# Kernel tuning notes

Measured on AMD Instinct MI355X. Metric: run time of the kernel, lower is better.

## Reference

```python
import math
import jax, jax.numpy as jnp
import numpy as np

N_HEADS = 16

def setup_inputs() -> dict:
    key = jax.random.key(0)
    k1, k2, k3 = jax.random.split(key, 3)
    B, S, D = 2, 2048, 1024
    x = jax.random.normal(k1, (B, S, D), dtype=jnp.float32)
    W_qkv = jax.random.normal(k2, (3 * D, D), dtype=jnp.float32)
    W_o = jax.random.normal(k3, (D, D), dtype=jnp.float32)
    return {"x": x, "W_qkv": W_qkv, "W_o": W_o}


def reference(x, W_qkv, W_o):
    B, S, D = x.shape
    H = N_HEADS
    d_h = D // H
    # fused QKV projection: (B,S,3D)
    t = jnp.matmul(x, W_qkv.T)
    t = t.reshape(B, S, 3, D)
    # NOTE: module reshapes (B,S,D) -> (B,H,S,d_h) directly (no transpose);
    # heads partition the flattened seq*feature layout. Replicate exactly.
    q = t[:, :, 0, :].reshape(B, H, S, d_h)
    k = t[:, :, 1, :].reshape(B, H, S, d_h)
    v = t[:, :, 2, :].reshape(B, H, S, d_h)
    # scaled by sqrt(d_model), as in the original (not sqrt(d_h))
    scores = jnp.einsum('bhqd,bhkd->bhqk', q, k) / math.sqrt(D)
    scores = jnp.tril(scores)
    # original sets ALL exact zeros to -inf (masks upper triangle)
    scores = jnp.where(scores == 0, -jnp.inf, scores)
    attn = jax.nn.softmax(scores, axis=-1)
    y_prime = jnp.matmul(attn, v)  # (B,H,S,d_h)
    y_prime = y_prime.transpose(0, 2, 1, 3).reshape(B, S, D)
    y = jnp.matmul(y_prime, W_o.T)
    return y
```

## Files before the change

kernel.cpp:

```cpp
#include <hip/hip_runtime.h>
#include <hip/hip_bf16.h>


using bf16 = __hip_bfloat16;
typedef __attribute__((ext_vector_type(8))) short bf16x8v;
typedef __attribute__((ext_vector_type(4))) float f32x4;

#define MFMA_BF16(A, B, C) __builtin_amdgcn_mfma_f32_16x16x32_bf16((A), (B), (C), 0, 0, 0)

#define GLD_LDS16(g, l)                                                        \
  __builtin_amdgcn_global_load_lds(                                            \
      (const __attribute__((address_space(1))) void*)(g),                      \
      (__attribute__((address_space(3))) void*)(l), 16, 0, 0)

static __device__ __forceinline__ unsigned short bf_bits(float f) {
  bf16 b = __float2bfloat16(f);
  return *reinterpret_cast<unsigned short*>(&b);
}

__global__ __launch_bounds__(256) void cvt_split(const float* __restrict__ in,
                                                 bf16* __restrict__ hi,
                                                 bf16* __restrict__ lo, int n) {
  int i = (blockIdx.x * 256 + threadIdx.x) * 4;
  if (i >= n) return;
  const float4 v = *(const float4*)(in + i);
  float vv[4] = {v.x, v.y, v.z, v.w};
  ushort4 hb, lb;
  unsigned short* hp = &hb.x;
  unsigned short* lp = &lb.x;
#pragma unroll
  for (int j = 0; j < 4; ++j) {
    bf16 h = __float2bfloat16(vv[j]);
    float r = vv[j] - __bfloat162float(h);
    hp[j] = bf_bits(vv[j]);
    lp[j] = bf_bits(r);
  }
  *(ushort4*)(hi + i) = hb;
  *(ushort4*)(lo + i) = lb;
}

__global__ __launch_bounds__(256) void cvt_plain(const float* __restrict__ in,
                                                 bf16* __restrict__ out, int n) {
  int i = (blockIdx.x * 256 + threadIdx.x) * 4;
  if (i >= n) return;
  const float4 v = *(const float4*)(in + i);
  ushort4 ob;
  ob.x = bf_bits(v.x); ob.y = bf_bits(v.y); ob.z = bf_bits(v.z); ob.w = bf_bits(v.w);
  *(ushort4*)(out + i) = ob;
}

__global__ __launch_bounds__(256) void gemm_qkv(
    const bf16* __restrict__ Ah, const bf16* __restrict__ Al,
    const bf16* __restrict__ Bh, const bf16* __restrict__ Bl,
    bf16* __restrict__ Qhi, bf16* __restrict__ Qlo,
    bf16* __restrict__ Khi, bf16* __restrict__ Klo,
    bf16* __restrict__ Vt) {
  const int K = 1024;
  const int NT = 24;
  __shared__ __attribute__((aligned(16))) bf16 AsH[2][4096], AsL[2][4096],
                                               BsH[2][4096], BsL[2][4096];
  const int t = threadIdx.x;
  const int lane = t & 63;
  const int wave = t >> 6;
  const int wr = wave >> 1, wc = wave & 1;
  int bid = blockIdx.x;
  bid = (bid & 7) * (768 >> 3) + (bid >> 3);
  const int bm = bid / NT, bn = bid % NT;
  const int brow = bm * 128, bcol = bn * 128;
  const bool isV = (bcol >= 2048);
  const bf16* pAh = Ah + (size_t)brow * K;
  const bf16* pAl = Al + (size_t)brow * K;
  const bf16* pBh = Bh + (size_t)bcol * K;
  const bf16* pBl = Bl + (size_t)bcol * K;
  const int r0 = t >> 2;
  const int c0 = (t & 3) * 8;
  f32x4 acc[4][4] = {};

#define STAGE(buf, k0_)                                                        \
  {                                                                            \
    const int _k = (k0_);                                                      \
    GLD_LDS16(pAh + (size_t)r0 * K + _k + c0,        &AsH[buf][t * 8]);        \
    GLD_LDS16(pAh + (size_t)(r0 + 64) * K + _k + c0, &AsH[buf][2048 + t * 8]); \
    GLD_LDS16(pBh + (size_t)r0 * K + _k + c0,        &BsH[buf][t * 8]);        \
    GLD_LDS16(pBh + (size_t)(r0 + 64) * K + _k + c0, &BsH[buf][2048 + t * 8]); \
    if (!isV) {                                                                \
      GLD_LDS16(pAl + (size_t)r0 * K + _k + c0,        &AsL[buf][t * 8]);      \
      GLD_LDS16(pAl + (size_t)(r0 + 64) * K + _k + c0, &AsL[buf][2048 + t * 8]);\
      GLD_LDS16(pBl + (size_t)r0 * K + _k + c0,        &BsL[buf][t * 8]);      \
      GLD_LDS16(pBl + (size_t)(r0 + 64) * K + _k + c0, &BsL[buf][2048 + t * 8]);\
    }                                                                          \
  }

  STAGE(0, 0);
  const int ao = (wr * 64 + (lane & 15)) * 32 + (lane >> 4) * 8;
  const int bo = (wc * 64 + (lane & 15)) * 32 + (lane >> 4) * 8;
  for (int tk = 0; tk < 32; ++tk) {
    const int cur = tk & 1;
    if (tk < 31) {
      STAGE(cur ^ 1, (tk + 1) * 32);
      if (!isV) asm volatile("s_waitcnt vmcnt(8)" ::: "memory");
      else      asm volatile("s_waitcnt vmcnt(4)" ::: "memory");
    } else {
      asm volatile("s_waitcnt vmcnt(0)" ::: "memory");
    }
    __builtin_amdgcn_sched_barrier(0);
    __builtin_amdgcn_s_barrier();
    asm volatile("" ::: "memory");
    bf16x8v ah[4], bh_[4];
#pragma unroll
    for (int i = 0; i < 4; ++i) {
      ah[i]  = *(const bf16x8v*)&AsH[cur][ao + i * 512];
      bh_[i] = *(const bf16x8v*)&BsH[cur][bo + i * 512];
    }
    if (!isV) {
      bf16x8v al[4], bl_[4];
#pragma unroll
      for (int i = 0; i < 4; ++i) {
        al[i]  = *(const bf16x8v*)&AsL[cur][ao + i * 512];
        bl_[i] = *(const bf16x8v*)&BsL[cur][bo + i * 512];
      }
#pragma unroll
      for (int i = 0; i < 4; ++i)
#pragma unroll
        for (int j = 0; j < 4; ++j) {
          acc[i][j] = MFMA_BF16(ah[i], bh_[j], acc[i][j]);
          acc[i][j] = MFMA_BF16(ah[i], bl_[j], acc[i][j]);
          acc[i][j] = MFMA_BF16(al[i], bh_[j], acc[i][j]);
        }
    } else {
#pragma unroll
      for (int i = 0; i < 4; ++i)
#pragma unroll
        for (int j = 0; j < 4; ++j)
          acc[i][j] = MFMA_BF16(ah[i], bh_[j], acc[i][j]);
    }
    asm volatile("" ::: "memory");
    __builtin_amdgcn_sched_barrier(0);
    __builtin_amdgcn_s_barrier();
    asm volatile("" ::: "memory");
  }
#undef STAGE
#pragma unroll
  for (int i = 0; i < 4; ++i)
#pragma unroll
    for (int j = 0; j < 4; ++j)
#pragma unroll
      for (int e = 0; e < 4; ++e) {
        const int m = brow + wr * 64 + i * 16 + ((lane >> 4) << 2) + e;
        const int n = bcol + wc * 64 + j * 16 + (lane & 15);
        float v = acc[i][j][e];
        const int b = m >> 11, s = m & 2047;
        const int c = n >> 10, d = n & 1023;
        const int bh_i = (b << 4) | (s >> 7);
        const int s2 = ((s & 127) << 4) | (d >> 6);
        const int dh = d & 63;
        if (c == 2) {
          Vt[((size_t)bh_i << 17) | ((size_t)dh << 11) | (size_t)s2] = __float2bfloat16(v);
        } else {
          if (c == 0) v *= 0.03125f;
          const size_t idx = ((size_t)bh_i << 17) | ((size_t)s2 << 6) | (size_t)dh;
          bf16 hv = __float2bfloat16(v);
          bf16 lv = __float2bfloat16(v - __bfloat162float(hv));
          if (c == 0) { Qhi[idx] = hv; Qlo[idx] = lv; }
          else        { Khi[idx] = hv; Klo[idx] = lv; }
        }
      }
}

__global__ __launch_bounds__(128, 2) void attn_kernel(
    const bf16* __restrict__ Qhi, const bf16* __restrict__ Qlo,
    const bf16* __restrict__ Khi, const bf16* __restrict__ Klo,
    const bf16* __restrict__ Vt, bf16* __restrict__ Yp) {
  const int lane = threadIdx.x & 63;
  const int wv   = threadIdx.x >> 6;
  const int bh = blockIdx.x & 31;
  const int c  = 63 - (blockIdx.x >> 5);
  const int b = bh >> 4, h = bh & 15;
  const size_t base = (size_t)bh << 17;
  const bf16* qh_p = Qhi + base;
  const bf16* ql_p = Qlo + base;
  const bf16* kh_p = Khi + base;
  const bf16* kl_p = Klo + base;
  const bf16* v_p  = Vt + base;
  const int qbase = c << 5;
  const int l15 = lane & 15;
  const int lg  = lane >> 4;

  __shared__ __attribute__((aligned(16))) float Xch[64][44];
  bf16* Plds = reinterpret_cast<bf16*>(&Xch[0][0]) + wv * 2304;

  bf16x8v qfh[2][2], qfl[2][2];
#pragma unroll
  for (int q2 = 0; q2 < 2; ++q2)
#pragma unroll
    for (int x2 = 0; x2 < 2; ++x2) {
      const size_t o = (size_t)(qbase + q2 * 16 + l15) * 64 + x2 * 32 + lg * 8;
      qfh[q2][x2] = *(const bf16x8v*)(qh_p + o);
      qfl[q2][x2] = *(const bf16x8v*)(ql_p + o);
    }
  bf16x8v ones8;
#pragma unroll
  for (int j = 0; j < 8; ++j) ones8[j] = (short)0x3F80;

  f32x4 oac[2][4] = {};
  f32x4 oden[2] = {};
  float mrun[2] = {-3.0e38f, -3.0e38f};
  const float L2E = 1.4426950408889634f;
  const int n  = (c >> 1) + 1;
  const int h0 = (n + 1) >> 1;
  const int kt0 = wv ? h0 : 0;
  const int kt1 = wv ? n : h0;
  const int diag = n - 1;

  for (int kt = kt0; kt < kt1; ++kt) {
    const int kb = kt << 6;
    f32x4 st[4][2] = {};
#pragma unroll
    for (int kf = 0; kf < 4; ++kf) {
      const size_t ko = (size_t)(kb + kf * 16 + l15) * 64 + lg * 8;
      const bf16x8v kh0 = *(const bf16x8v*)(kh_p + ko);
      const bf16x8v kh1 = *(const bf16x8v*)(kh_p + ko + 32);
      const bf16x8v kl0 = *(const bf16x8v*)(kl_p + ko);
      const bf16x8v kl1 = *(const bf16x8v*)(kl_p + ko + 32);
#pragma unroll
      for (int q2 = 0; q2 < 2; ++q2) {
        f32x4 a = st[kf][q2];
        a = MFMA_BF16(kh0, qfh[q2][0], a);
        a = MFMA_BF16(kh1, qfh[q2][1], a);
        a = MFMA_BF16(kh0, qfl[q2][0], a);
        a = MFMA_BF16(kh1, qfl[q2][1], a);
        a = MFMA_BF16(kl0, qfh[q2][0], a);
        a = MFMA_BF16(kl1, qfh[q2][1], a);
        st[kf][q2] = a;
      }
    }
    if (kt == diag) {
#pragma unroll
      for (int kf = 0; kf < 4; ++kf)
#pragma unroll
        for (int q2 = 0; q2 < 2; ++q2)
#pragma unroll
          for (int e = 0; e < 4; ++e) {
            const int key = kb + kf * 16 + (lg << 2) + e;
            const int qr  = qbase + q2 * 16 + l15;
            if (key > qr) st[kf][q2][e] = -3.0e38f;
          }
    }
    float tmax[2] = {-3.0e38f, -3.0e38f};
#pragma unroll
    for (int kf = 0; kf < 4; ++kf)
#pragma unroll
      for (int q2 = 0; q2 < 2; ++q2)
#pragma unroll
        for (int e = 0; e < 4; ++e)
          tmax[q2] = fmaxf(tmax[q2], st[kf][q2][e]);
#pragma unroll
    for (int q2 = 0; q2 < 2; ++q2) {
      tmax[q2] = fmaxf(tmax[q2], __shfl_xor(tmax[q2], 16));
      tmax[q2] = fmaxf(tmax[q2], __shfl_xor(tmax[q2], 32));
    }
    const int ok = (tmax[0] <= mrun[0] + 8.0f) && (tmax[1] <= mrun[1] + 8.0f);
    if (!__all(ok)) {
      float sfac[2];
#pragma unroll
      for (int q2 = 0; q2 < 2; ++q2) {
        const float mn = fmaxf(mrun[q2], tmax[q2]);
        sfac[q2] = exp2f((mrun[q2] - mn) * L2E);
        mrun[q2] = mn;
      }
#pragma unroll
      for (int q2 = 0; q2 < 2; ++q2)
#pragma unroll
        for (int e = 0; e < 4; ++e) {
          const float so = __shfl(sfac[q2], (lg << 2) + e);
          oden[q2][e] *= so;
#pragma unroll
          for (int df = 0; df < 4; ++df) oac[q2][df][e] *= so;
        }
    }
    const float mL0 = mrun[0] * L2E, mL1 = mrun[1] * L2E;
#pragma unroll
    for (int kf = 0; kf < 4; ++kf)
#pragma unroll
      for (int q2 = 0; q2 < 2; ++q2) {
        const float mL = q2 ? mL1 : mL0;
        ushort4 pk;
        unsigned short* pp = &pk.x;
#pragma unroll
        for (int e = 0; e < 4; ++e)
          pp[e] = bf_bits(exp2f(fmaf(st[kf][q2][e], L2E, -mL)));
        *(ushort4*)(Plds + (q2 * 16 + l15) * 72 + kf * 16 + (lg << 2)) = pk;
      }
    bf16x8v vreg[2][4];
#pragma unroll
    for (int x2 = 0; x2 < 2; ++x2)
#pragma unroll
      for (int df = 0; df < 4; ++df)
        vreg[x2][df] =
            *(const bf16x8v*)(v_p + (size_t)(df * 16 + l15) * 2048 + kb + x2 * 32 + lg * 8);
    asm volatile("s_waitcnt lgkmcnt(0)" ::: "memory");
    __builtin_amdgcn_sched_barrier(0);
    bf16x8v pa[2][2];
#pragma unroll
    for (int x2 = 0; x2 < 2; ++x2)
#pragma unroll
      for (int q2 = 0; q2 < 2; ++q2)
        pa[x2][q2] = *(const bf16x8v*)(Plds + (q2 * 16 + l15) * 72 + x2 * 32 + lg * 8);
    asm volatile("" ::: "memory");
#pragma unroll
    for (int x2 = 0; x2 < 2; ++x2) {
#pragma unroll
      for (int q2 = 0; q2 < 2; ++q2)
        oden[q2] = MFMA_BF16(pa[x2][q2], ones8, oden[q2]);
#pragma unroll
      for (int df = 0; df < 4; ++df)
#pragma unroll
        for (int q2 = 0; q2 < 2; ++q2)
          oac[q2][df] = MFMA_BF16(pa[x2][q2], vreg[x2][df], oac[q2][df]);
    }
  }

  __syncthreads();
  if (wv == 1) {
    float* dst = &Xch[lane][0];
    dst[0] = mrun[0];
    dst[1] = mrun[1];
#pragma unroll
    for (int q2 = 0; q2 < 2; ++q2)
#pragma unroll
      for (int e = 0; e < 4; ++e) dst[2 + q2 * 4 + e] = oden[q2][e];
#pragma unroll
    for (int q2 = 0; q2 < 2; ++q2)
#pragma unroll
      for (int df = 0; df < 4; ++df)
#pragma unroll
        for (int e = 0; e < 4; ++e)
          dst[10 + q2 * 16 + df * 4 + e] = oac[q2][df][e];
  }
  __syncthreads();
  if (wv == 0) {
    const float* src = &Xch[lane][0];
#pragma unroll
    for (int q2 = 0; q2 < 2; ++q2) {
      const float m1 = src[q2];
      const float mm = fmaxf(mrun[q2], m1);
      const float f0c = exp2f((mrun[q2] - mm) * L2E);
      const float f1c = exp2f((m1 - mm) * L2E);
#pragma unroll
      for (int e = 0; e < 4; ++e) {
        const float f0 = __shfl(f0c, (lg << 2) + e);
        const float f1 = __shfl(f1c, (lg << 2) + e);
        oden[q2][e] = oden[q2][e] * f0 + src[2 + q2 * 4 + e] * f1;
#pragma unroll
        for (int df = 0; df < 4; ++df)
          oac[q2][df][e] = oac[q2][df][e] * f0 + src[10 + q2 * 16 + df * 4 + e] * f1;
      }
    }
#pragma unroll
    for (int q2 = 0; q2 < 2; ++q2) {
      float li[4];
#pragma unroll
      for (int e = 0; e < 4; ++e) li[e] = 1.0f / oden[q2][e];
#pragma unroll
      for (int df = 0; df < 4; ++df)
#pragma unroll
        for (int e = 0; e < 4; ++e) {
          const int qr = qbase + q2 * 16 + (lg << 2) + e;
          const int dh = df * 16 + l15;
          Yp[(size_t)(b * 2048 + qr) * 1024 + h * 64 + dh] =
              __float2bfloat16(oac[q2][df][e] * li[e]);
        }
    }
  }
}

__global__ __launch_bounds__(256) void gemm_out(const bf16* __restrict__ A,
                                                const bf16* __restrict__ B,
                                                float* __restrict__ C) {
  const int K = 1024;
  const int NT = 8;
  __shared__ __attribute__((aligned(16))) bf16 As[2048], Bs[4096];
  const int t = threadIdx.x;
  const int lane = t & 63;
  const int wave = t >> 6;
  const int wr = wave >> 1, wc = wave & 1;
  int bid = blockIdx.x;
  bid = (bid & 7) * (512 >> 3) + (bid >> 3);
  const int bm = bid / NT, bn = bid % NT;
  const int brow = bm * 64, bcol = bn * 128;
  const bf16* pA = A + (size_t)brow * K;
  const bf16* pB = B + (size_t)bcol * K;
  const int r0 = t >> 2;
  const int c0 = (t & 3) * 8;
  f32x4 acc[2][4] = {};
  for (int k0 = 0; k0 < K; k0 += 32) {
    __syncthreads();
    GLD_LDS16(pA + (size_t)r0 * K + k0 + c0,        &As[t * 8]);
    GLD_LDS16(pB + (size_t)r0 * K + k0 + c0,        &Bs[t * 8]);
    GLD_LDS16(pB + (size_t)(r0 + 64) * K + k0 + c0, &Bs[2048 + t * 8]);
    __syncthreads();
    bf16x8v af[2], bf_[4];
    const int l15 = lane & 15, lg = lane >> 4;
#pragma unroll
    for (int i = 0; i < 2; ++i)
      af[i] = *(const bf16x8v*)&As[(wr * 32 + i * 16 + l15) * 32 + lg * 8];
#pragma unroll
    for (int j = 0; j < 4; ++j) {
      const int rB = wc * 64 + j * 16 + l15;
      bf_[j] = *(const bf16x8v*)&Bs[(rB & 63) * 32 + (rB >> 6) * 2048 + lg * 8];
    }
#pragma unroll
    for (int i = 0; i < 2; ++i)
#pragma unroll
      for (int j = 0; j < 4; ++j)
        acc[i][j] = MFMA_BF16(af[i], bf_[j], acc[i][j]);
  }
#pragma unroll
  for (int i = 0; i < 2; ++i)
#pragma unroll
    for (int j = 0; j < 4; ++j)
#pragma unroll
      for (int e = 0; e < 4; ++e) {
        const int m = brow + wr * 32 + i * 16 + ((lane >> 4) << 2) + e;
        const int n = bcol + wc * 64 + j * 16 + (lane & 15);
        C[(size_t)m * 1024 + n] = acc[i][j][e];
      }
}

extern "C" void kernel_launch(void* const* d_in, const int* in_sizes, int n_in,
                              void* d_out, int out_size, void* d_ws, size_t ws_size,
                              hipStream_t stream) {
  (void)in_sizes; (void)n_in; (void)out_size; (void)ws_size;
  const float* x    = (const float*)d_in[0];
  const float* wqkv = (const float*)d_in[1];
  const float* wo   = (const float*)d_in[2];
  float* out = (float*)d_out;

  const size_t NX = 4096ull * 1024;
  const size_t NW = 3072ull * 1024;
  const size_t NO = 1024ull * 1024;

  bf16* p = (bf16*)d_ws;
  bf16* xh  = p; p += NX;
  bf16* xl  = p; p += NX;
  bf16* wqh = p; p += NW;
  bf16* wql = p; p += NW;
  bf16* wob = p; p += NO;
  bf16* qhi = p; p += NX;
  bf16* qlo = p; p += NX;
  bf16* khi = p; p += NX;
  bf16* klo = p; p += NX;
  bf16* vt  = p; p += NX;
  bf16* yp  = p; p += NX;

  hipLaunchKernelGGL(cvt_split, dim3(NX / 1024), dim3(256), 0, stream, x, xh, xl, (int)NX);
  hipLaunchKernelGGL(cvt_split, dim3(NW / 1024), dim3(256), 0, stream, wqkv, wqh, wql, (int)NW);
  hipLaunchKernelGGL(cvt_plain, dim3(NO / 1024), dim3(256), 0, stream, wo, wob, (int)NO);
  hipLaunchKernelGGL(gemm_qkv, dim3(32 * 24), dim3(256), 0, stream,
                     xh, xl, wqh, wql, qhi, qlo, khi, klo, vt);
  hipLaunchKernelGGL(attn_kernel, dim3(2048), dim3(128), 0, stream,
                     qhi, qlo, khi, klo, vt, yp);
  hipLaunchKernelGGL(gemm_out, dim3(64 * 8), dim3(256), 0, stream, yp, wob, out);
}
```

Measured before the change: 313.1 us.

## Swizzle LDS tiles in QKV and output GEMMs, drop QKV double buffering

```diff
diff --git a/kernel.cpp b/kernel.cpp
--- a/kernel.cpp
+++ b/kernel.cpp
@@ -57,8 +57,7 @@
     bf16* __restrict__ Vt) {
   const int K = 1024;
   const int NT = 24;
-  __shared__ __attribute__((aligned(16))) bf16 AsH[2][4096], AsL[2][4096],
-                                               BsH[2][4096], BsL[2][4096];
+  __shared__ __attribute__((aligned(16))) bf16 AsH[4096], AsL[4096], BsH[4096], BsL[4096];
   const int t = threadIdx.x;
   const int lane = t & 63;
   const int wave = t >> 6;
@@ -73,51 +72,38 @@
   const bf16* pBh = Bh + (size_t)bcol * K;
   const bf16* pBl = Bl + (size_t)bcol * K;
   const int r0 = t >> 2;
-  const int c0 = (t & 3) * 8;
+  const int c0 = (((t & 3) ^ ((t >> 3) & 3))) * 8;
   f32x4 acc[4][4] = {};
-
-#define STAGE(buf, k0_)                                                        \
-  {                                                                            \
-    const int _k = (k0_);                                                      \
-    GLD_LDS16(pAh + (size_t)r0 * K + _k + c0,        &AsH[buf][t * 8]);        \
-    GLD_LDS16(pAh + (size_t)(r0 + 64) * K + _k + c0, &AsH[buf][2048 + t * 8]); \
-    GLD_LDS16(pBh + (size_t)r0 * K + _k + c0,        &BsH[buf][t * 8]);        \
-    GLD_LDS16(pBh + (size_t)(r0 + 64) * K + _k + c0, &BsH[buf][2048 + t * 8]); \
-    if (!isV) {                                                                \
-      GLD_LDS16(pAl + (size_t)r0 * K + _k + c0,        &AsL[buf][t * 8]);      \
-      GLD_LDS16(pAl + (size_t)(r0 + 64) * K + _k + c0, &AsL[buf][2048 + t * 8]);\
-      GLD_LDS16(pBl + (size_t)r0 * K + _k + c0,        &BsL[buf][t * 8]);      \
-      GLD_LDS16(pBl + (size_t)(r0 + 64) * K + _k + c0, &BsL[buf][2048 + t * 8]);\
-    }                                                                          \
-  }
-
-  STAGE(0, 0);
-  const int ao = (wr * 64 + (lane & 15)) * 32 + (lane >> 4) * 8;
-  const int bo = (wc * 64 + (lane & 15)) * 32 + (lane >> 4) * 8;
-  for (int tk = 0; tk < 32; ++tk) {
-    const int cur = tk & 1;
-    if (tk < 31) {
-      STAGE(cur ^ 1, (tk + 1) * 32);
-      if (!isV) asm volatile("s_waitcnt vmcnt(8)" ::: "memory");
-      else      asm volatile("s_waitcnt vmcnt(4)" ::: "memory");
-    } else {
-      asm volatile("s_waitcnt vmcnt(0)" ::: "memory");
-    }
-    __builtin_amdgcn_sched_barrier(0);
-    __builtin_amdgcn_s_barrier();
-    asm volatile("" ::: "memory");
+  const int l15 = lane & 15;
+  const int lg  = lane >> 4;
+  const int cxor = (l15 >> 1) & 3;
+  const int ao = (wr * 64 + l15) * 32 + ((lg ^ cxor)) * 8;
+  const int bo = (wc * 64 + l15) * 32 + ((lg ^ cxor)) * 8;
+  for (int k0 = 0; k0 < K; k0 += 32) {
+    __syncthreads();
+    GLD_LDS16(pAh + (size_t)r0 * K + k0 + c0,        &AsH[t * 8]);
+    GLD_LDS16(pAh + (size_t)(r0 + 64) * K + k0 + c0, &AsH[2048 + t * 8]);
+    GLD_LDS16(pBh + (size_t)r0 * K + k0 + c0,        &BsH[t * 8]);
+    GLD_LDS16(pBh + (size_t)(r0 + 64) * K + k0 + c0, &BsH[2048 + t * 8]);
+    if (!isV) {
+      GLD_LDS16(pAl + (size_t)r0 * K + k0 + c0,        &AsL[t * 8]);
+      GLD_LDS16(pAl + (size_t)(r0 + 64) * K + k0 + c0, &AsL[2048 + t * 8]);
+      GLD_LDS16(pBl + (size_t)r0 * K + k0 + c0,        &BsL[t * 8]);
+      GLD_LDS16(pBl + (size_t)(r0 + 64) * K + k0 + c0, &BsL[2048 + t * 8]);
+    }
+    __syncthreads();
     bf16x8v ah[4], bh_[4];
 #pragma unroll
     for (int i = 0; i < 4; ++i) {
-      ah[i]  = *(const bf16x8v*)&AsH[cur][ao + i * 512];
-      bh_[i] = *(const bf16x8v*)&BsH[cur][bo + i * 512];
+      ah[i]  = *(const bf16x8v*)&AsH[ao + i * 512];
+      bh_[i] = *(const bf16x8v*)&BsH[bo + i * 512];
     }
     if (!isV) {
       bf16x8v al[4], bl_[4];
 #pragma unroll
       for (int i = 0; i < 4; ++i) {
-        al[i]  = *(const bf16x8v*)&AsL[cur][ao + i * 512];
-        bl_[i] = *(const bf16x8v*)&BsL[cur][bo + i * 512];
+        al[i]  = *(const bf16x8v*)&AsL[ao + i * 512];
+        bl_[i] = *(const bf16x8v*)&BsL[bo + i * 512];
       }
 #pragma unroll
       for (int i = 0; i < 4; ++i)
@@ -134,12 +120,7 @@
         for (int j = 0; j < 4; ++j)
           acc[i][j] = MFMA_BF16(ah[i], bh_[j], acc[i][j]);
     }
-    asm volatile("" ::: "memory");
-    __builtin_amdgcn_sched_barrier(0);
-    __builtin_amdgcn_s_barrier();
-    asm volatile("" ::: "memory");
-  }
-#undef STAGE
+  }
 #pragma unroll
   for (int i = 0; i < 4; ++i)
 #pragma unroll
@@ -391,7 +372,9 @@
   const bf16* pA = A + (size_t)brow * K;
   const bf16* pB = B + (size_t)bcol * K;
   const int r0 = t >> 2;
-  const int c0 = (t & 3) * 8;
+  const int c0 = (((t & 3) ^ ((t >> 3) & 3))) * 8;
+  const int l15 = lane & 15, lg = lane >> 4;
+  const int cxor = (l15 >> 1) & 3;
   f32x4 acc[2][4] = {};
   for (int k0 = 0; k0 < K; k0 += 32) {
     __syncthreads();
@@ -400,14 +383,13 @@
     GLD_LDS16(pB + (size_t)(r0 + 64) * K + k0 + c0, &Bs[2048 + t * 8]);
     __syncthreads();
     bf16x8v af[2], bf_[4];
-    const int l15 = lane & 15, lg = lane >> 4;
 #pragma unroll
     for (int i = 0; i < 2; ++i)
-      af[i] = *(const bf16x8v*)&As[(wr * 32 + i * 16 + l15) * 32 + lg * 8];
+      af[i] = *(const bf16x8v*)&As[(wr * 32 + i * 16 + l15) * 32 + (lg ^ cxor) * 8];
 #pragma unroll
     for (int j = 0; j < 4; ++j) {
       const int rB = wc * 64 + j * 16 + l15;
-      bf_[j] = *(const bf16x8v*)&Bs[(rB & 63) * 32 + (rB >> 6) * 2048 + lg * 8];
+      bf_[j] = *(const bf16x8v*)&Bs[(rB & 63) * 32 + (rB >> 6) * 2048 + (lg ^ cxor) * 8];
     }
 #pragma unroll
     for (int i = 0; i < 2; ++i)
```

Result: faster. 305.8 us (-2.3%).
